# Optimization experiments

Hardware: AMD Instinct MI355X
Metric: run time of the kernel (lower is better)

Reference implementation:

```python
import jax, jax.numpy as jnp
import numpy as np

MASK_FILL = -987654321.0


def rotate_every_two(x):
    # pairs (x0, x1) -> (-x1, x0), interleaved back along last dim
    x1 = x[..., 0::2]
    x2 = x[..., 1::2]
    return jnp.stack((-x2, x1), axis=-1).reshape(x.shape)


def setup_inputs() -> dict:
    key = jax.random.key(0)
    ks = jax.random.split(key, 6)
    b, n, dim = 64, 197, 768
    heads, dim_head = 12, 64
    inner = heads * dim_head
    x = jax.random.normal(ks[0], (b, n, dim), dtype=jnp.float32)
    pos_emb = jax.random.normal(ks[1], (1, n, dim_head), dtype=jnp.float32)
    w_qkv = jax.random.normal(ks[2], (dim, 3 * inner), dtype=jnp.float32) * (dim ** -0.5)
    scale = jnp.full((heads,), dim_head ** -0.5, dtype=jnp.float32)
    w_out = jax.random.normal(ks[3], (inner, dim), dtype=jnp.float32) * (inner ** -0.5)
    b_out = jnp.zeros((dim,), dtype=jnp.float32)
    return {"x": x, "pos_emb": pos_emb, "w_qkv": w_qkv, "scale": scale,
            "w_out": w_out, "b_out": b_out}


def reference(x, pos_emb, w_qkv, scale, w_out, b_out):
    b, n, dim = x.shape
    h = scale.shape[0]
    qkv = x @ w_qkv                         # [b, n, 3*inner]
    q, k, v = jnp.split(qkv, 3, axis=-1)
    dh = q.shape[-1] // h
    to_heads = lambda t: t.reshape(b, n, h, dh).transpose(0, 2, 1, 3)  # bhnd
    q, k, v = to_heads(q), to_heads(k), to_heads(v)

    # RoPE: pos_emb [1, n, (2 * dh/2)] -> sin/cos [n, dh/2] -> interleave to [n, dh]
    sc = pos_emb[0].reshape(n, 2, dh // 2)
    sin = jnp.repeat(sc[:, 0], 2, axis=-1)  # [n, dh]
    cos = jnp.repeat(sc[:, 1], 2, axis=-1)
    q = q * cos + rotate_every_two(q) * sin
    k = k * cos + rotate_every_two(k) * sin

    # per-head learnable scale
    dots = jnp.einsum('bhid,bhjd->bhij', q, k) * scale[None, :, None, None]
    # diagonal (LSA) mask
    eye = jnp.eye(n, dtype=bool)
    dots = jnp.where(eye, MASK_FILL, dots)

    attn = jax.nn.softmax(dots, axis=-1)
    out = jnp.einsum('bhij,bhjd->bhid', attn, v)
    out = out.transpose(0, 2, 1, 3).reshape(b, n, h * dh)
    return out @ w_out + b_out
```

## Files before the change

### kernel.cpp

```cpp
#include <hip/hip_runtime.h>
#include <math.h>

#define MASK_FILL_F (-987654321.0f)

typedef unsigned short u16;
typedef unsigned int   u32;

constexpr int Bb   = 64;
constexpr int Ntok = 197;
constexpr int Dim  = 768;
constexpr int Heads= 12;
constexpr int Dh   = 64;
constexpr int Nq3  = 2304;
constexpr int Rows = 12608;
constexpr int Mpad = 12672;

using f32x4  = __attribute__((ext_vector_type(4))) float;
using bf16x8 = __attribute__((ext_vector_type(8))) short;

__device__ __forceinline__ u16 f2bf(float f) {
  u32 u = __float_as_uint(f);
  u = (u + 0x7fffu + ((u >> 16) & 1u)) >> 16;
  return (u16)u;
}

__device__ __forceinline__ void stage16(const void* gp, void* lp) {
  __builtin_amdgcn_global_load_lds(
      (const __attribute__((address_space(1))) u32*)gp,
      (__attribute__((address_space(3))) u32*)lp, 16, 0, 0);
}

__device__ __forceinline__ int sigma6(int M) {
  return (M & 0x23) | (((M >> 3) & 1) << 4) | (((M >> 2) & 1) << 3) |
         (((M >> 4) & 1) << 2);
}

__global__ __launch_bounds__(256) void cvt_bf16(const float* __restrict__ in,
                                                u16* __restrict__ out, int n4) {
  const int i = blockIdx.x * 256 + threadIdx.x;
  if (i < n4) {
    const float4 v = *(const float4*)&in[(size_t)i * 4];
    ushort4 u;
    u.x = f2bf(v.x); u.y = f2bf(v.y); u.z = f2bf(v.z); u.w = f2bf(v.w);
    *(ushort4*)&out[(size_t)i * 4] = u;
  }
}

__global__ __launch_bounds__(256) void transpose_cvt(const float* __restrict__ in,
                                                     u16* __restrict__ out,
                                                     int R, int C) {
  __shared__ float t[32][33];
  const int c0 = blockIdx.x * 32, r0 = blockIdx.y * 32;
  const int tx = threadIdx.x & 31, ty = threadIdx.x >> 5;
#pragma unroll
  for (int rr = ty; rr < 32; rr += 8)
    t[rr][tx] = in[(size_t)(r0 + rr) * C + c0 + tx];
  __syncthreads();
#pragma unroll
  for (int cc = ty; cc < 32; cc += 8)
    out[(size_t)(c0 + cc) * R + r0 + tx] = f2bf(t[tx][cc]);
}

__global__ __launch_bounds__(256) void vtrans(const u16* __restrict__ qkvB,
                                              u16* __restrict__ vT) {
  __shared__ u16 t[64 * 72];
  const int jt = blockIdx.x, bh = blockIdx.y;
  const int b = bh / Heads, h = bh % Heads;
  const int j0 = jt * 64;
  const int tid = threadIdx.x;

  for (int idx = tid; idx < 512; idx += 256) {
    const int jr = idx >> 3, c8 = (idx & 7) * 8;
    const int j = j0 + jr;
    uint4 u = make_uint4(0u, 0u, 0u, 0u);
    if (j < Ntok)
      u = *(const uint4*)(qkvB + (size_t)(b * Ntok + j) * Nq3 + 2 * Dim + h * Dh + c8);
    *(uint4*)&t[jr * 72 + c8] = u;
  }
  __syncthreads();
  for (int idx = tid; idx < 512; idx += 256) {
    const int d = idx >> 3, j8 = (idx & 7) * 8;
    ushort4 lo, hi;
    lo.x = t[(j8 + 0) * 72 + d]; lo.y = t[(j8 + 1) * 72 + d];
    lo.z = t[(j8 + 2) * 72 + d]; lo.w = t[(j8 + 3) * 72 + d];
    hi.x = t[(j8 + 4) * 72 + d]; hi.y = t[(j8 + 5) * 72 + d];
    hi.z = t[(j8 + 6) * 72 + d]; hi.w = t[(j8 + 7) * 72 + d];
    u16* dst = vT + ((size_t)bh * 64 + d) * 256 + j0 + j8;
    *(ushort4*)dst       = lo;
    *(ushort4*)(dst + 4) = hi;
  }
}

constexpr int Kc  = 768;
constexpr int NKT = Kc / 64;

#define BARM() asm volatile("s_barrier" ::: "memory")
#define VMW4() asm volatile("s_waitcnt vmcnt(4)" ::: "memory")

#define STGA(chunk, kt, BUF) \
  stage16(Ag + (size_t)(m0 + (chunk) * 8 + srow) * Kc + (kt) * 64 + scol, \
          &As[BUF][(chunk) * 512])
#define STGB(chunk, kt, BUF) \
  stage16(Bg + (size_t)(n0 + (chunk) * 8 + srow) * Kc + (kt) * 64 + scol, \
          &Bs[BUF][(chunk) * 512])

#define RDA(BUF, MH) \
  _Pragma("unroll") for (int m_ = 0; m_ < 4; ++m_) \
  _Pragma("unroll") for (int k_ = 0; k_ < 2; ++k_) \
    af[m_][k_] = *(const bf16x8*)&As[BUF][(wr * 128 + (MH) * 64 + m_ * 16 + tx) * 64 \
                                          + (((k_ * 4 + qd) ^ sx) * 8)];
#define RDB(BUF, NH, BFR) \
  _Pragma("unroll") for (int n_ = 0; n_ < 2; ++n_) \
  _Pragma("unroll") for (int k_ = 0; k_ < 2; ++k_) \
    BFR[n_][k_] = *(const bf16x8*)&Bs[BUF][(wc * 64 + (NH) * 32 + n_ * 16 + tx) * 64 \
                                           + (((k_ * 4 + qd) ^ sx) * 8)];

#define MM(MH, NH, BFR) \
  __builtin_amdgcn_s_setprio(1); \
  _Pragma("unroll") for (int m_ = 0; m_ < 4; ++m_) \
  _Pragma("unroll") for (int n_ = 0; n_ < 2; ++n_) \
  _Pragma("unroll") for (int k_ = 0; k_ < 2; ++k_) \
    acc[(MH) * 4 + m_][(NH) * 2 + n_] = __builtin_amdgcn_mfma_f32_16x16x32_bf16( \
        af[m_][k_], BFR[n_][k_], acc[(MH) * 4 + m_][(NH) * 2 + n_], 0, 0, 0); \
  __builtin_amdgcn_s_setprio(0);

template<int MODE, int TN>
__global__ __launch_bounds__(512, 2) void gemm8p(
    const u16* __restrict__ Ag, const u16* __restrict__ Bg,
    void* __restrict__ Cv, int Nn, int nwg,
    const float* __restrict__ pe, const float* __restrict__ bias)
{
  __shared__ u16 As[2][256 * 64];
  __shared__ u16 Bs[2][256 * 64];

  const int tid = threadIdx.x, lane = tid & 63, w = tid >> 6;

  const int orig = blockIdx.x;
  const int q8 = nwg >> 3, r8 = nwg & 7;
  const int xcd = orig & 7, sub = orig >> 3;
  const int wgid = (xcd < r8 ? xcd * (q8 + 1) : r8 * (q8 + 1) + (xcd - r8) * q8) + sub;
  const int tm = wgid / TN, tn = wgid % TN;
  const int m0 = tm * 256, n0 = tn * 256;

  const int wr = w >> 2, wc = w & 3;
  const int tx = lane & 15, qd = lane >> 4, sx = tx & 7;

  const int srow = lane >> 3;
  const int scol = ((lane & 7) ^ srow) * 8;
  const int b0 = (w >> 1) * 8 + (w & 1) * 2;

  STGA(w, 0, 0);        STGA(16 + w, 0, 0);
  STGB(b0 + 4, 0, 0);   STGB(b0 + 5, 0, 0);
  STGA(8 + w, 0, 0);    STGA(24 + w, 0, 0);
  STGB(b0, 0, 0);       STGB(b0 + 1, 0, 0);
  STGA(w, 1, 1);        STGA(16 + w, 1, 1);
  STGB(b0 + 4, 1, 1);   STGB(b0 + 5, 1, 1);
  VMW4();
  BARM();

  f32x4  acc[8][4] = {};
  bf16x8 af[4][2], bf0[2][2], bf1[2][2];

#pragma unroll 1
  for (int i = 0; i < NKT / 2; ++i) {
    const int u = 2 * i;
    RDA(0, 0); RDB(0, 0, bf0);
    STGA(8 + w, u + 1, 1); STGA(24 + w, u + 1, 1);
    BARM(); MM(0, 0, bf0); BARM();
    RDB(0, 1, bf1);
    STGB(b0, u + 1, 1); STGB(b0 + 1, u + 1, 1);
    BARM(); MM(0, 1, bf1); BARM();
    RDA(0, 1);
    STGA(w, u + 2, 0); STGA(16 + w, u + 2, 0);
    BARM(); MM(1, 1, bf1); BARM();
    STGB(b0 + 4, u + 2, 0); STGB(b0 + 5, u + 2, 0);
    BARM(); MM(1, 0, bf0); VMW4(); BARM();
    RDA(1, 0); RDB(1, 0, bf0);
    STGA(8 + w, u + 2, 0); STGA(24 + w, u + 2, 0);
    BARM(); MM(0, 0, bf0); BARM();
    RDB(1, 1, bf1);
    STGB(b0, u + 2, 0); STGB(b0 + 1, u + 2, 0);
    BARM(); MM(0, 1, bf1); BARM();
    RDA(1, 1);
    STGA(w, u + 3, 1); STGA(16 + w, u + 3, 1);
    BARM(); MM(1, 1, bf1); BARM();
    STGB(b0 + 4, u + 3, 1); STGB(b0 + 5, u + 3, 1);
    BARM(); MM(1, 0, bf0); VMW4(); BARM();
  }

  if (MODE == 0) {
    u16* C = (u16*)Cv;
    const bool dorot = (n0 < 2 * Dim);
#pragma unroll
    for (int mi = 0; mi < 8; ++mi) {
      const int rbase = m0 + wr * 128 + mi * 16 + qd * 4;
      int iq[4];
#pragma unroll
      for (int r = 0; r < 4; ++r) iq[r] = (rbase + r) % Ntok;
#pragma unroll
      for (int ni = 0; ni < 4; ++ni) {
        const int col = n0 + wc * 64 + ni * 16 + tx;
        const int mm  = (col & 63) >> 1;
        const int odd = col & 1;
#pragma unroll
        for (int r = 0; r < 4; ++r) {
          float v = acc[mi][ni][r];
          float res = v;
          if (dorot) {
            const float other = __shfl_xor(v, 1, 64);
            const float sn = pe[iq[r] * 64 + mm];
            const float c2 = pe[iq[r] * 64 + 32 + mm];
            res = odd ? (v * c2 + other * sn) : (v * c2 - other * sn);
          }
          C[(size_t)(rbase + r) * Nn + col] = f2bf(res);
        }
      }
    }
  } else {
    float* C = (float*)Cv;
#pragma unroll
    for (int mi = 0; mi < 8; ++mi) {
      const int rbase = m0 + wr * 128 + mi * 16 + qd * 4;
#pragma unroll
      for (int ni = 0; ni < 4; ++ni) {
        const int col = n0 + wc * 64 + ni * 16 + tx;
        const float bv = bias[col];
#pragma unroll
        for (int r = 0; r < 4; ++r) {
          const int row = rbase + r;
          if (row < Rows) C[(size_t)row * Nn + col] = acc[mi][ni][r] + bv;
        }
      }
    }
  }
}

constexpr int LS = 72;

__global__ __launch_bounds__(256) void attn7(
    const u16* __restrict__ qkvB, const u16* __restrict__ vT,
    const float* __restrict__ scale, u16* __restrict__ outB)
{
  __shared__ u16 ks [64 * LS];
  __shared__ u16 vts[64 * LS];

  const int it = blockIdx.x, bh = blockIdx.y;
  const int b = bh / Heads, h = bh % Heads;
  const int i0 = it * 128;
  const float sc = scale[h];
  const int tid = threadIdx.x, lane = tid & 63, w = tid >> 6;
  const int tx = lane & 15, q = lane >> 4;
  const size_t rowbase = (size_t)b * Ntok;

  bf16x8 bq[2][2];
#pragma unroll
  for (int g = 0; g < 2; ++g)
#pragma unroll
    for (int kk = 0; kk < 2; ++kk)
      bq[g][kk] = *(const bf16x8*)(qkvB +
          (rowbase + i0 + 32 * w + 16 * g + tx) * (size_t)Nq3 + h * Dh + kk * 32 + q * 8);

  float l_part[2] = {0.f, 0.f};
  f32x4 oacc[2][4] = {};

  for (int jt = 0; jt < 4; ++jt) {
    const int j0 = jt * 64;
    __syncthreads();

    for (int idx = tid; idx < 512; idx += 256) {
      const int M = idx >> 3, c8 = (idx & 7) * 8;
      const int js = sigma6(M);
      *(uint4*)&ks[M * LS + c8] =
          *(const uint4*)(qkvB + (rowbase + j0 + js) * (size_t)Nq3 + Dim + h * Dh + c8);
    }
    for (int idx = tid; idx < 512; idx += 256) {
      const int d = idx >> 3, c8 = (idx & 7) * 8;
      *(uint4*)&vts[d * LS + c8] =
          *(const uint4*)(vT + ((size_t)bh * 64 + d) * 256 + j0 + c8);
    }
    __syncthreads();

#pragma unroll
    for (int g = 0; g < 2; ++g) {
      f32x4 sT[4] = {};
#pragma unroll
      for (int kk = 0; kk < 2; ++kk)
#pragma unroll
        for (int jb = 0; jb < 4; ++jb) {
          const bf16x8 ka = *(const bf16x8*)&ks[(jb * 16 + tx) * LS + kk * 32 + q * 8];
          sT[jb] = __builtin_amdgcn_mfma_f32_16x16x32_bf16(ka, bq[g][kk], sT[jb], 0, 0, 0);
        }

      const int ig = i0 + 32 * w + 16 * g + tx;
      union { bf16x8 v; u16 e[8]; } pk[2];
      float lp = 0.f;
#pragma unroll
      for (int jb = 0; jb < 4; ++jb)
#pragma unroll
        for (int r = 0; r < 4; ++r) {
          const int jg = j0 + 32 * (jb >> 1) + 8 * q + 4 * (jb & 1) + r;
          const float s = fminf(sT[jb][r] * sc, 80.f);
          const bool bad = (jg >= Ntok) || (jg == ig);
          const float p = bad ? 0.f : __expf(s);
          lp += p;
          pk[jb >> 1].e[(jb & 1) * 4 + r] = f2bf(p);
        }
      l_part[g] += lp;

#pragma unroll
      for (int kk = 0; kk < 2; ++kk)
#pragma unroll
        for (int nb = 0; nb < 4; ++nb) {
          const bf16x8 vb = *(const bf16x8*)&vts[(nb * 16 + tx) * LS + kk * 32 + q * 8];
          oacc[g][nb] = __builtin_amdgcn_mfma_f32_16x16x32_bf16(pk[kk].v, vb,
                                                               oacc[g][nb], 0, 0, 0);
        }
    }
  }

#pragma unroll
  for (int g = 0; g < 2; ++g) {
    float l = l_part[g];
    l += __shfl_xor(l, 16, 64);
    l += __shfl_xor(l, 32, 64);
    const float linv = 1.0f / l;
#pragma unroll
    for (int r = 0; r < 4; ++r) {
      const float lr = __shfl(linv, 4 * q + r, 64);
      const int igr = i0 + 32 * w + 16 * g + 4 * q + r;
      if (igr < Ntok) {
#pragma unroll
        for (int nb = 0; nb < 4; ++nb)
          outB[(rowbase + igr) * (size_t)Dim + h * Dh + nb * 16 + tx] =
              f2bf(oacc[g][nb][r] * lr);
      }
    }
  }
}

extern "C" void kernel_launch(void* const* d_in, const int* in_sizes, int n_in,
                              void* d_out, int out_size, void* d_ws, size_t ws_size,
                              hipStream_t stream) {
  const float* x     = (const float*)d_in[0];
  const float* pe    = (const float*)d_in[1];
  const float* w_qkv = (const float*)d_in[2];
  const float* scale = (const float*)d_in[3];
  const float* w_out = (const float*)d_in[4];
  const float* b_out = (const float*)d_in[5];
  float* out = (float*)d_out;

  u16* xb    = (u16*)d_ws;
  u16* wqkvT = xb    + (size_t)Mpad * Dim;
  u16* woutT = wqkvT + (size_t)Nq3 * Dim;
  u16* qkvB  = woutT + (size_t)Dim * Dim;
  u16* attnB = qkvB  + (size_t)Mpad * Nq3;
  u16* vT    = attnB + (size_t)Mpad * Dim;

  cvt_bf16<<<(Rows * Dim / 4 + 255) / 256, 256, 0, stream>>>(x, xb, Rows * Dim / 4);
  transpose_cvt<<<dim3(Nq3 / 32, Dim / 32), 256, 0, stream>>>(w_qkv, wqkvT, Dim, Nq3);
  transpose_cvt<<<dim3(Dim / 32, Dim / 32), 256, 0, stream>>>(w_out, woutT, Dim, Dim);

  constexpr int NWG0 = 50 * 9;
  gemm8p<0, 9><<<NWG0, 512, 0, stream>>>(xb, wqkvT, qkvB, Nq3, NWG0, pe, nullptr);

  vtrans<<<dim3(4, Bb * Heads), 256, 0, stream>>>(qkvB, vT);

  attn7<<<dim3(2, Bb * Heads), 256, 0, stream>>>(qkvB, vT, scale, attnB);

  constexpr int NWG1 = 50 * 3;
  gemm8p<1, 3><<<NWG1, 512, 0, stream>>>(attnB, woutT, out, Dim, NWG1, nullptr, b_out);
}
```

Before: 282.9 us.

## Merge attention query tiles per head, prefetch K/V, use simpler output GEMM

Attention now launches one 512-thread block per batch-head instead of two 256-thread blocks. Each thread loads its K/V tile slice into registers and prefetches the next tile while the current one is computed, which cuts the redundant K/V loads the two query blocks used to make. The output projection moves from the 256x256 pipelined GEMM (150 workgroups) to a simple 128x128 tiled MFMA GEMM with more blocks, to fill more CUs. The pipelined GEMM also clamps prefetch k-tile indices so it no longer loads past the end of K. Risks are less latency hiding in the plain GEMM and fewer attention blocks in flight.

```diff
diff --git a/kernel.cpp b/kernel.cpp
--- a/kernel.cpp
+++ b/kernel.cpp
@@ -93,6 +93,7 @@
 
 constexpr int Kc  = 768;
 constexpr int NKT = Kc / 64;
+#define KTC(x) ((x) < NKT ? (x) : (NKT - 1))
 
 #define BARM() asm volatile("s_barrier" ::: "memory")
 #define VMW4() asm volatile("s_waitcnt vmcnt(4)" ::: "memory")
@@ -124,11 +125,11 @@
         af[m_][k_], BFR[n_][k_], acc[(MH) * 4 + m_][(NH) * 2 + n_], 0, 0, 0); \
   __builtin_amdgcn_s_setprio(0);
 
-template<int MODE, int TN>
+template<int TN>
 __global__ __launch_bounds__(512, 2) void gemm8p(
     const u16* __restrict__ Ag, const u16* __restrict__ Bg,
-    void* __restrict__ Cv, int Nn, int nwg,
-    const float* __restrict__ pe, const float* __restrict__ bias)
+    u16* __restrict__ Cb, int Nn, int nwg,
+    const float* __restrict__ pe)
 {
   __shared__ u16 As[2][256 * 64];
   __shared__ u16 Bs[2][256 * 64];
@@ -171,65 +172,99 @@
     STGB(b0, u + 1, 1); STGB(b0 + 1, u + 1, 1);
     BARM(); MM(0, 1, bf1); BARM();
     RDA(0, 1);
-    STGA(w, u + 2, 0); STGA(16 + w, u + 2, 0);
+    STGA(w, KTC(u + 2), 0); STGA(16 + w, KTC(u + 2), 0);
     BARM(); MM(1, 1, bf1); BARM();
-    STGB(b0 + 4, u + 2, 0); STGB(b0 + 5, u + 2, 0);
+    STGB(b0 + 4, KTC(u + 2), 0); STGB(b0 + 5, KTC(u + 2), 0);
     BARM(); MM(1, 0, bf0); VMW4(); BARM();
     RDA(1, 0); RDB(1, 0, bf0);
-    STGA(8 + w, u + 2, 0); STGA(24 + w, u + 2, 0);
+    STGA(8 + w, KTC(u + 2), 0); STGA(24 + w, KTC(u + 2), 0);
     BARM(); MM(0, 0, bf0); BARM();
     RDB(1, 1, bf1);
-    STGB(b0, u + 2, 0); STGB(b0 + 1, u + 2, 0);
+    STGB(b0, KTC(u + 2), 0); STGB(b0 + 1, KTC(u + 2), 0);
     BARM(); MM(0, 1, bf1); BARM();
     RDA(1, 1);
-    STGA(w, u + 3, 1); STGA(16 + w, u + 3, 1);
+    STGA(w, KTC(u + 3), 1); STGA(16 + w, KTC(u + 3), 1);
     BARM(); MM(1, 1, bf1); BARM();
-    STGB(b0 + 4, u + 3, 1); STGB(b0 + 5, u + 3, 1);
+    STGB(b0 + 4, KTC(u + 3), 1); STGB(b0 + 5, KTC(u + 3), 1);
     BARM(); MM(1, 0, bf0); VMW4(); BARM();
   }
 
-  if (MODE == 0) {
-    u16* C = (u16*)Cv;
-    const bool dorot = (n0 < 2 * Dim);
-#pragma unroll
-    for (int mi = 0; mi < 8; ++mi) {
-      const int rbase = m0 + wr * 128 + mi * 16 + qd * 4;
-      int iq[4];
-#pragma unroll
-      for (int r = 0; r < 4; ++r) iq[r] = (rbase + r) % Ntok;
-#pragma unroll
-      for (int ni = 0; ni < 4; ++ni) {
-        const int col = n0 + wc * 64 + ni * 16 + tx;
-        const int mm  = (col & 63) >> 1;
-        const int odd = col & 1;
-#pragma unroll
-        for (int r = 0; r < 4; ++r) {
-          float v = acc[mi][ni][r];
-          float res = v;
-          if (dorot) {
-            const float other = __shfl_xor(v, 1, 64);
-            const float sn = pe[iq[r] * 64 + mm];
-            const float c2 = pe[iq[r] * 64 + 32 + mm];
-            res = odd ? (v * c2 + other * sn) : (v * c2 - other * sn);
-          }
-          C[(size_t)(rbase + r) * Nn + col] = f2bf(res);
+  const bool dorot = (n0 < 2 * Dim);
+#pragma unroll
+  for (int mi = 0; mi < 8; ++mi) {
+    const int rbase = m0 + wr * 128 + mi * 16 + qd * 4;
+    int iq[4];
+#pragma unroll
+    for (int r = 0; r < 4; ++r) iq[r] = (rbase + r) % Ntok;
+#pragma unroll
+    for (int ni = 0; ni < 4; ++ni) {
+      const int col = n0 + wc * 64 + ni * 16 + tx;
+      const int mm  = (col & 63) >> 1;
+      const int odd = col & 1;
+#pragma unroll
+      for (int r = 0; r < 4; ++r) {
+        float v = acc[mi][ni][r];
+        float res = v;
+        if (dorot) {
+          const float other = __shfl_xor(v, 1, 64);
+          const float sn = pe[iq[r] * 64 + mm];
+          const float c2 = pe[iq[r] * 64 + 32 + mm];
+          res = odd ? (v * c2 + other * sn) : (v * c2 - other * sn);
         }
+        Cb[(size_t)(rbase + r) * Nn + col] = f2bf(res);
       }
     }
-  } else {
-    float* C = (float*)Cv;
-#pragma unroll
-    for (int mi = 0; mi < 8; ++mi) {
-      const int rbase = m0 + wr * 128 + mi * 16 + qd * 4;
-#pragma unroll
-      for (int ni = 0; ni < 4; ++ni) {
-        const int col = n0 + wc * 64 + ni * 16 + tx;
-        const float bv = bias[col];
-#pragma unroll
-        for (int r = 0; r < 4; ++r) {
-          const int row = rbase + r;
-          if (row < Rows) C[(size_t)row * Nn + col] = acc[mi][ni][r] + bv;
-        }
+  }
+}
+
+__global__ __launch_bounds__(256) void gemm_bt1(
+    const u16* __restrict__ Ag, const u16* __restrict__ Bg,
+    float* __restrict__ C, int K, int Nn, const float* __restrict__ bias)
+{
+  __shared__ u16 As[128 * 32];
+  __shared__ u16 Bs[128 * 32];
+  const int tid = threadIdx.x, lane = tid & 63, w = tid >> 6;
+  const int m0 = blockIdx.y * 128, n0 = blockIdx.x * 128;
+  const int wm = (w & 1) * 64, wn = (w >> 1) * 64;
+  const int tx = lane & 15, qk = lane >> 4;
+  const int rs = lane >> 2, cs = (lane & 3) * 8;
+
+  f32x4 acc[4][4] = {};
+
+  for (int k0 = 0; k0 < K; k0 += 32) {
+#pragma unroll
+    for (int t = 0; t < 2; ++t) {
+      const int r0 = w * 16 + t * 64;
+      stage16(Ag + (size_t)(m0 + r0 + rs) * K + k0 + cs, &As[r0 * 32]);
+      stage16(Bg + (size_t)(n0 + r0 + rs) * K + k0 + cs, &Bs[r0 * 32]);
+    }
+    __syncthreads();
+    bf16x8 af[4], bf[4];
+#pragma unroll
+    for (int f = 0; f < 4; ++f) {
+      af[f] = *(const bf16x8*)&As[(wm + f * 16 + tx) * 32 + qk * 8];
+      bf[f] = *(const bf16x8*)&Bs[(wn + f * 16 + tx) * 32 + qk * 8];
+    }
+#pragma unroll
+    for (int fm = 0; fm < 4; ++fm)
+#pragma unroll
+      for (int fn = 0; fn < 4; ++fn)
+        acc[fm][fn] = __builtin_amdgcn_mfma_f32_16x16x32_bf16(
+            af[fm], bf[fn], acc[fm][fn], 0, 0, 0);
+    __syncthreads();
+  }
+
+#pragma unroll
+  for (int fm = 0; fm < 4; ++fm) {
+    const int rbase = m0 + wm + fm * 16 + qk * 4;
+#pragma unroll
+    for (int fn = 0; fn < 4; ++fn) {
+      const int col = n0 + wn + fn * 16 + tx;
+      const float bv = bias[col];
+#pragma unroll
+      for (int r = 0; r < 4; ++r) {
+        const int row = rbase + r;
+        if (row < Rows) C[(size_t)row * Nn + col] = acc[fm][fn][r] + bv;
       }
     }
   }
@@ -237,28 +272,34 @@
 
 constexpr int LS = 72;
 
-__global__ __launch_bounds__(256) void attn7(
+__global__ __launch_bounds__(512) void attn8(
     const u16* __restrict__ qkvB, const u16* __restrict__ vT,
     const float* __restrict__ scale, u16* __restrict__ outB)
 {
   __shared__ u16 ks [64 * LS];
   __shared__ u16 vts[64 * LS];
 
-  const int it = blockIdx.x, bh = blockIdx.y;
+  const int bh = blockIdx.x;
   const int b = bh / Heads, h = bh % Heads;
-  const int i0 = it * 128;
   const float sc = scale[h];
   const int tid = threadIdx.x, lane = tid & 63, w = tid >> 6;
   const int tx = lane & 15, q = lane >> 4;
   const size_t rowbase = (size_t)b * Ntok;
 
+  const int Ms = tid >> 3, c8s = (tid & 7) * 8;
+  const u16* kgp = qkvB + (rowbase + sigma6(Ms)) * (size_t)Nq3 + Dim + h * Dh + c8s;
+  const u16* vgp = vT + ((size_t)bh * 64 + Ms) * 256 + c8s;
+
   bf16x8 bq[2][2];
 #pragma unroll
   for (int g = 0; g < 2; ++g)
 #pragma unroll
     for (int kk = 0; kk < 2; ++kk)
       bq[g][kk] = *(const bf16x8*)(qkvB +
-          (rowbase + i0 + 32 * w + 16 * g + tx) * (size_t)Nq3 + h * Dh + kk * 32 + q * 8);
+          (rowbase + 32 * w + 16 * g + tx) * (size_t)Nq3 + h * Dh + kk * 32 + q * 8);
+
+  uint4 kreg = *(const uint4*)kgp;
+  uint4 vreg = *(const uint4*)vgp;
 
   float l_part[2] = {0.f, 0.f};
   f32x4 oacc[2][4] = {};
@@ -266,19 +307,13 @@
   for (int jt = 0; jt < 4; ++jt) {
     const int j0 = jt * 64;
     __syncthreads();
-
-    for (int idx = tid; idx < 512; idx += 256) {
-      const int M = idx >> 3, c8 = (idx & 7) * 8;
-      const int js = sigma6(M);
-      *(uint4*)&ks[M * LS + c8] =
-          *(const uint4*)(qkvB + (rowbase + j0 + js) * (size_t)Nq3 + Dim + h * Dh + c8);
-    }
-    for (int idx = tid; idx < 512; idx += 256) {
-      const int d = idx >> 3, c8 = (idx & 7) * 8;
-      *(uint4*)&vts[d * LS + c8] =
-          *(const uint4*)(vT + ((size_t)bh * 64 + d) * 256 + j0 + c8);
-    }
+    *(uint4*)&ks [Ms * LS + c8s] = kreg;
+    *(uint4*)&vts[Ms * LS + c8s] = vreg;
     __syncthreads();
+    if (jt < 3) {
+      kreg = *(const uint4*)(kgp + (size_t)(jt + 1) * 64 * Nq3);
+      vreg = *(const uint4*)(vgp + (jt + 1) * 64);
+    }
 
 #pragma unroll
     for (int g = 0; g < 2; ++g) {
@@ -291,7 +326,7 @@
           sT[jb] = __builtin_amdgcn_mfma_f32_16x16x32_bf16(ka, bq[g][kk], sT[jb], 0, 0, 0);
         }
 
-      const int ig = i0 + 32 * w + 16 * g + tx;
+      const int ig = 32 * w + 16 * g + tx;
       union { bf16x8 v; u16 e[8]; } pk[2];
       float lp = 0.f;
 #pragma unroll
@@ -327,7 +362,7 @@
 #pragma unroll
     for (int r = 0; r < 4; ++r) {
       const float lr = __shfl(linv, 4 * q + r, 64);
-      const int igr = i0 + 32 * w + 16 * g + 4 * q + r;
+      const int igr = 32 * w + 16 * g + 4 * q + r;
       if (igr < Ntok) {
 #pragma unroll
         for (int nb = 0; nb < 4; ++nb)
@@ -361,12 +396,12 @@
   transpose_cvt<<<dim3(Dim / 32, Dim / 32), 256, 0, stream>>>(w_out, woutT, Dim, Dim);
 
   constexpr int NWG0 = 50 * 9;
-  gemm8p<0, 9><<<NWG0, 512, 0, stream>>>(xb, wqkvT, qkvB, Nq3, NWG0, pe, nullptr);
+  gemm8p<9><<<NWG0, 512, 0, stream>>>(xb, wqkvT, qkvB, Nq3, NWG0, pe);
 
   vtrans<<<dim3(4, Bb * Heads), 256, 0, stream>>>(qkvB, vT);
 
-  attn7<<<dim3(2, Bb * Heads), 256, 0, stream>>>(qkvB, vT, scale, attnB);
-
-  constexpr int NWG1 = 50 * 3;
-  gemm8p<1, 3><<<NWG1, 512, 0, stream>>>(attnB, woutT, out, Dim, NWG1, nullptr, b_out);
-}
+  attn8<<<Bb * Heads, 512, 0, stream>>>(qkvB, vT, scale, attnB);
+
+  gemm_bt1<<<dim3(Dim / 128, Mpad / 128), 256, 0, stream>>>(
+      attnB, woutT, out, Dim, Dim, b_out);
+}
```

After: 273.4 us. -3.3%, faster.
